# Performance work log

Measured on AMD Instinct MI355X. Metric: run time of the kernel, lower is better.

Reference implementation:

```python
import jax, jax.numpy as jnp
import numpy as np

B, T, C, H, N = 4, 4096, 2048, 32, 64
DMIX, DDEC = 32, 64
N_LAYER, LAYER_ID = 24, 12
GN_EPS = 1e-5 * 8.0 ** 2  # eps = 1e-5 * head_size_divisor**2


def setup_inputs() -> dict:
    key = jax.random.key(0)
    ks = jax.random.split(key, 24)
    r01 = LAYER_ID / (N_LAYER - 1)
    r1a0 = 1.0 - LAYER_ID / N_LAYER
    ddd = (np.arange(C, dtype=np.float32) / C).reshape(1, 1, C)
    maa = lambda p: jnp.asarray(1.0 - ddd ** p, dtype=jnp.float32)
    # decay speed schedule (canonical RWKV6, over channel dim)
    n = np.arange(C, dtype=np.float32)
    decay = (-6.0 + 5.0 * (n / (C - 1)) ** (0.7 + 1.3 * r01)).reshape(1, 1, C)
    # time_faaaa zigzag schedule
    m = np.arange(C, dtype=np.float32)
    zig = ((m + 1) % 3 - 1) * 0.1
    faaaa = (r01 * (1 - m / (C - 1)) + zig).reshape(H, N)
    s = 1.0 / np.sqrt(C)
    return {
        "x": jax.random.normal(ks[0], (B, T, C), jnp.float32),
        "shift_state": jax.random.normal(ks[1], (B, C), jnp.float32),
        "wkv_state": jnp.zeros((B, H, N, N), jnp.float32),
        "time_maa_x": maa(r1a0),
        "time_maa_w": maa(r1a0),
        "time_maa_k": maa(r1a0),
        "time_maa_v": jnp.asarray(1.0 - (ddd ** r1a0 + 0.3 * r01), jnp.float32),
        "time_maa_r": maa(0.5 * r1a0),
        "time_maa_g": maa(0.5 * r1a0),
        "time_maa_w1": jax.random.normal(ks[2], (C, 5 * DMIX), jnp.float32) * 0.01,
        "time_maa_w2": jax.random.uniform(ks[3], (5, DMIX, C), jnp.float32, -0.01, 0.01),
        "time_decay": jnp.asarray(decay, jnp.float32),
        "time_decay_w1": jax.random.normal(ks[4], (C, DDEC), jnp.float32) * 0.01,
        "time_decay_w2": jax.random.uniform(ks[5], (DDEC, C), jnp.float32, -0.01, 0.01),
        "time_faaaa": jnp.asarray(faaaa, jnp.float32),
        "Wr": jax.random.normal(ks[6], (C, C), jnp.float32) * s,
        "Wk": jax.random.normal(ks[7], (C, C), jnp.float32) * s,
        "Wv": jax.random.normal(ks[8], (C, C), jnp.float32) * s,
        "Wg": jax.random.normal(ks[9], (C, C), jnp.float32) * s,
        "Wo": jax.random.normal(ks[10], (C, C), jnp.float32) * s,
        "gn_weight": jnp.ones((C,), jnp.float32),
        "gn_bias": jnp.zeros((C,), jnp.float32),
    }


def reference(x, shift_state, wkv_state, time_maa_x, time_maa_w, time_maa_k,
              time_maa_v, time_maa_r, time_maa_g, time_maa_w1, time_maa_w2,
              time_decay, time_decay_w1, time_decay_w2, time_faaaa,
              Wr, Wk, Wv, Wg, Wo, gn_weight, gn_bias):
    b, t, c = x.shape
    # token shift: previous token (seeded by shift_state) minus current
    xx = jnp.concatenate([shift_state[:, None, :], x[:, :-1]], axis=1) - x
    lx = x[:, -1]
    # LoRA token-shift mixing
    xxx = x + xx * time_maa_x
    t5 = jnp.tanh(xxx @ time_maa_w1).reshape(b, t, 5, DMIX)
    mixes = jnp.einsum('btfd,fdc->fbtc', t5, time_maa_w2)
    mw, mk, mv, mr, mg = mixes
    xw = x + xx * (time_maa_w + mw)
    xk = x + xx * (time_maa_k + mk)
    xv = x + xx * (time_maa_v + mv)
    xr = x + xx * (time_maa_r + mr)
    xg = x + xx * (time_maa_g + mg)
    r = xr @ Wr
    k = xk @ Wk
    v = xv @ Wv
    g = jax.nn.silu(xg @ Wg)
    # data-dependent decay via LoRA; wkv6 uses log-decay -exp(w)
    w = time_decay + jnp.tanh(xw @ time_decay_w1) @ time_decay_w2
    glog = -jnp.exp(w)  # [b,t,c]
    to_heads = lambda z: z.reshape(b, t, H, N).transpose(1, 0, 2, 3)  # [t,b,h,n]
    rh, kh, vh, gh = to_heads(r), to_heads(k), to_heads(v), to_heads(glog)
    u = time_faaaa  # [H,N]

    def step(S, inp):
        r_t, k_t, v_t, g_t = inp  # each [b,h,n]
        kv = jnp.einsum('bhk,bhv->bhkv', k_t, v_t)
        o_t = jnp.einsum('bhk,bhkv->bhv', r_t, S + u[None, :, :, None] * kv)
        S = jnp.exp(g_t)[..., None] * S + kv
        return S, o_t

    state, o = jax.lax.scan(step, wkv_state, (rh, kh, vh, gh))
    o = o.transpose(1, 0, 2, 3).reshape(b, t, c)  # [b,t,c]
    # GroupNorm with H groups over channel dim
    og = o.reshape(b, t, H, N)
    mu = og.mean(-1, keepdims=True)
    var = og.var(-1, keepdims=True)
    on = (og - mu) * jax.lax.rsqrt(var + GN_EPS)
    on = on * gn_weight.reshape(H, N) + gn_bias.reshape(H, N)
    out = (on.reshape(b, t, c) * g) @ Wo
    return out, lx, state
```

## Files before the change

kernel.cpp:

```cpp
#include <hip/hip_runtime.h>
#include <hip/hip_bf16.h>
#include <stdint.h>

#define DEV __device__ __forceinline__

typedef __bf16 bf16x8 __attribute__((ext_vector_type(8)));
typedef float f32x4 __attribute__((ext_vector_type(4)));
typedef unsigned short u16x8 __attribute__((ext_vector_type(8)));

constexpr int kB = 4, kT = 4096, kC = 2048, kH = 32, kN = 64;
constexpr int kM = kB * kT;
constexpr int SEGN = 8, TSEG = kT / SEGN, CHN = TSEG / 64;

DEV float bfu2f(unsigned short u) {
  union { uint32_t i; float f; } x; x.i = ((uint32_t)u) << 16; return x.f;
}
DEV unsigned short f2bfu(float f) {
  union { float f; uint32_t i; } x; x.f = f;
  uint32_t r = x.i + 0x7FFFu + ((x.i >> 16) & 1u);
  return (unsigned short)(r >> 16);
}

DEV void gld16(const void* g, void* l) {
  __builtin_amdgcn_global_load_lds(
      (const __attribute__((address_space(1))) void*)g,
      (__attribute__((address_space(3))) void*)l, 16, 0, 0);
}

DEV int swzb(int row, int byteoff) { return (row << 7) + (byteoff ^ ((row & 7) << 4)); }
DEV int swz64(int row, int byteoff) { return (row << 6) + (byteoff ^ ((row & 3) << 4)); }

__global__ __launch_bounds__(256) void trans_bf16(
    const float* __restrict__ in, unsigned short* __restrict__ out, int R, int Cn) {
  __shared__ __attribute__((aligned(16))) unsigned short tile[64][65];
  const int t = threadIdx.x;
  const int r0 = blockIdx.y * 64, c0 = blockIdx.x * 64;
  const int lr = t >> 6, lc = t & 63;
#pragma unroll
  for (int i = 0; i < 16; i++) {
    int rr = lr + i * 4;
    int gr = r0 + rr, gc = c0 + lc;
    if (gr < R && gc < Cn) tile[rr][lc] = f2bfu(in[(size_t)gr * Cn + gc]);
  }
  __syncthreads();
#pragma unroll
  for (int i = 0; i < 16; i++) {
    int cc = lr + i * 4;
    int gc = c0 + cc, gr = r0 + lc;
    if (gc < Cn && gr < R) out[(size_t)gc * R + gr] = tile[lc][cc];
  }
}

__global__ __launch_bounds__(256) void prep_x2(
    const float* __restrict__ x, const float* __restrict__ shift,
    const float* __restrict__ maax,
    unsigned short* __restrict__ xxx, float* __restrict__ lx) {
  size_t i4 = ((size_t)blockIdx.x * 256 + threadIdx.x) * 4;
  int c = (int)(i4 & (kC - 1));
  size_t bt = i4 >> 11;
  int tt = (int)(bt & (kT - 1));
  int b = (int)(bt >> 12);
  float4 xv = *(const float4*)(x + i4);
  float4 pv = (tt == 0) ? *(const float4*)(shift + (size_t)b * kC + c)
                        : *(const float4*)(x + i4 - kC);
  float4 mx = *(const float4*)(maax + c);
  ushort4 o4;
  o4.x = f2bfu(xv.x + (pv.x - xv.x) * mx.x);
  o4.y = f2bfu(xv.y + (pv.y - xv.y) * mx.y);
  o4.z = f2bfu(xv.z + (pv.z - xv.z) * mx.z);
  o4.w = f2bfu(xv.w + (pv.w - xv.w) * mx.w);
  *(ushort4*)(xxx + i4) = o4;
  if (tt == kT - 1) *(float4*)(lx + (size_t)b * kC + c) = xv;
}

enum { E_F32 = 0, E_BF16 = 1, E_TANH = 2, E_SILU = 3 };

template <int BM, int BN, int EPI>
__global__ __launch_bounds__(256) void gemm_k(
    const unsigned short* __restrict__ A, const unsigned short* __restrict__ Bt,
    void* __restrict__ Cout, int M, int N, int K) {
  constexpr int WGM = (BM == 128 && BN == 128) ? 2 : (BM == 64 ? 2 : 4);
  constexpr int WGN = 4 / WGM;
  constexpr int WM = BM / WGM, WN = BN / WGN;
  constexpr int WR = WM / 16, WC = WN / 16;
  __shared__ __attribute__((aligned(16))) unsigned short As[BM * 32];
  __shared__ __attribute__((aligned(16))) unsigned short Bs[BN * 32];
  const int t = threadIdx.x, wid = t >> 6, l = t & 63;
  const int m0 = blockIdx.x * BM, n0 = blockIdx.y * BN;
  const int wm0 = (wid / WGN) * WM, wn0 = (wid % WGN) * WN;
  f32x4 acc[WR][WC];
#pragma unroll
  for (int i = 0; i < WR; i++)
#pragma unroll
    for (int j = 0; j < WC; j++) acc[i][j] = f32x4{0.f, 0.f, 0.f, 0.f};

  const int rowS = t >> 2, cbS = (t & 3) * 16;
  const char* Ab = (const char*)A;
  const char* Bb = (const char*)Bt;
  const int aoff = (wm0 + (l & 15)) * 32 + (l >> 4) * 8;
  const int boff = (wn0 + (l & 15)) * 32 + (l >> 4) * 8;

  for (int kt = 0; kt < K; kt += 32) {
#pragma unroll
    for (int ia = 0; ia < BM / 64; ia++)
      gld16(Ab + ((size_t)(m0 + ia * 64 + rowS) * K + kt) * 2 + cbS,
            (char*)As + ia * 4096 + wid * 1024);
    if constexpr (BN >= 64) {
#pragma unroll
      for (int ib = 0; ib < BN / 64; ib++)
        gld16(Bb + ((size_t)(n0 + ib * 64 + rowS) * K + kt) * 2 + cbS,
              (char*)Bs + ib * 4096 + wid * 1024);
    } else {
      if (t < BN * 4)
        gld16(Bb + ((size_t)(n0 + rowS) * K + kt) * 2 + cbS,
              (char*)Bs + wid * 1024);
    }
    __syncthreads();
    bf16x8 af[WR], bfv[WC];
#pragma unroll
    for (int mi = 0; mi < WR; mi++) af[mi] = *(const bf16x8*)(&As[aoff + mi * 512]);
#pragma unroll
    for (int ni = 0; ni < WC; ni++) bfv[ni] = *(const bf16x8*)(&Bs[boff + ni * 512]);
#pragma unroll
    for (int mi = 0; mi < WR; mi++)
#pragma unroll
      for (int ni = 0; ni < WC; ni++)
        acc[mi][ni] = __builtin_amdgcn_mfma_f32_16x16x32_bf16(af[mi], bfv[ni], acc[mi][ni], 0, 0, 0);
    __syncthreads();
  }

#pragma unroll
  for (int mi = 0; mi < WR; mi++) {
#pragma unroll
    for (int ni = 0; ni < WC; ni++) {
      int row = m0 + wm0 + mi * 16 + (l >> 4) * 4;
      int col = n0 + wn0 + ni * 16 + (l & 15);
#pragma unroll
      for (int j = 0; j < 4; j++) {
        float v = acc[mi][ni][j];
        size_t idx = (size_t)(row + j) * N + col;
        if constexpr (EPI == E_F32) ((float*)Cout)[idx] = v;
        else if constexpr (EPI == E_BF16) ((unsigned short*)Cout)[idx] = f2bfu(v);
        else if constexpr (EPI == E_TANH) ((unsigned short*)Cout)[idx] = f2bfu(tanhf(v));
        else if constexpr (EPI == E_SILU) ((unsigned short*)Cout)[idx] = f2bfu(v / (1.f + expf(-v)));
      }
    }
  }
}

template <int EPI>
__global__ __launch_bounds__(512, 2) void gemm256_k(
    const unsigned short* __restrict__ A, const unsigned short* __restrict__ Bt,
    void* __restrict__ Cout, int M, int N, int K) {
  extern __shared__ __attribute__((aligned(16))) char lds[];
  const int tid = threadIdx.x, wid = tid >> 6, l = tid & 63;
  const int fr = l & 15, fq = l >> 4;

  const int mtiles = M >> 8, ntiles = N >> 8;
  const int slab = mtiles >> 3;
  const int xcd = blockIdx.x & 7, loc = blockIdx.x >> 3;
  const int m0 = (xcd * slab + loc / ntiles) * 256;
  const int n0 = (loc % ntiles) * 256;

  const int wm = (wid >> 2) * 128, wn = (wid & 3) * 64;

  const int srow0 = tid >> 2;
  const int scb = ((tid & 3) * 16) ^ ((srow0 & 3) << 4);
  const char* pa2[2]; const char* pb2[2];
#pragma unroll
  for (int i = 0; i < 2; i++) {
    pa2[i] = (const char*)A + (size_t)(m0 + i * 128 + srow0) * K * 2 + scb;
    pb2[i] = (const char*)Bt + (size_t)(n0 + i * 128 + srow0) * K * 2 + scb;
  }

  const char* vA[8]; const char* vB[4];
#pragma unroll
  for (int mi = 0; mi < 8; mi++)
    vA[mi] = lds + swz64(wm + mi * 16 + fr, fq * 16);
#pragma unroll
  for (int ni = 0; ni < 4; ni++)
    vB[ni] = lds + 32768 + swz64(wn + ni * 16 + fr, fq * 16);

  f32x4 acc[8][4];
#pragma unroll
  for (int i = 0; i < 8; i++)
#pragma unroll
    for (int j = 0; j < 4; j++) acc[i][j] = f32x4{0.f, 0.f, 0.f, 0.f};

  auto STG = [&](int q, int s, int ktb) {
    const int d = q * 65536 + s * 16384 + wid * 1024;
    gld16(pa2[0] + ktb + s * 64, lds + d);
    gld16(pa2[1] + ktb + s * 64, lds + d + 8192);
    gld16(pb2[0] + ktb + s * 64, lds + 32768 + d);
    gld16(pb2[1] + ktb + s * 64, lds + 32768 + d + 8192);
  };

  auto PH = [&](int p, int s, bool doStage, int ktbNext, int vm) {
    if (vm)
      asm volatile("s_waitcnt vmcnt(4)" ::: "memory");
    else
      asm volatile("s_waitcnt vmcnt(0)" ::: "memory");
    __builtin_amdgcn_s_barrier();
    __builtin_amdgcn_sched_barrier(0);
    const int pb = p * 65536 + s * 16384;
    bf16x8 a[8], b[4];
#pragma unroll
    for (int mi = 0; mi < 8; mi++) a[mi] = *(const bf16x8*)(vA[mi] + pb);
#pragma unroll
    for (int ni = 0; ni < 4; ni++) b[ni] = *(const bf16x8*)(vB[ni] + pb);
    if (doStage) STG(p ^ 1, s, ktbNext);
    __builtin_amdgcn_sched_barrier(0);
    __builtin_amdgcn_s_setprio(1);
#pragma unroll
    for (int ni = 0; ni < 4; ni++)
#pragma unroll
      for (int mi = 0; mi < 8; mi++)
        acc[mi][ni] = __builtin_amdgcn_mfma_f32_16x16x32_bf16(a[mi], b[ni], acc[mi][ni], 0, 0, 0);
    __builtin_amdgcn_s_setprio(0);
  };

  const int KT = K >> 6;
  STG(0, 0, 0);
  STG(0, 1, 0);

  int T = 0;
  for (; T + 2 < KT; T += 2) {
    PH(0, 0, true, (T + 1) * 128, 4);
    PH(0, 1, true, (T + 1) * 128, 4);
    PH(1, 0, true, (T + 2) * 128, 4);
    PH(1, 1, true, (T + 2) * 128, 4);
  }
  PH(0, 0, true, (KT - 1) * 128, 4);
  PH(0, 1, true, (KT - 1) * 128, 4);
  PH(1, 0, false, 0, 4);
  PH(1, 1, false, 0, 0);

#pragma unroll
  for (int mi = 0; mi < 8; mi++)
#pragma unroll
    for (int ni = 0; ni < 4; ni++) {
      int row = m0 + wm + mi * 16 + fq * 4;
      int col = n0 + wn + ni * 16 + fr;
#pragma unroll
      for (int j = 0; j < 4; j++) {
        float v = acc[mi][ni][j];
        size_t idx = (size_t)(row + j) * N + col;
        if constexpr (EPI == E_F32) ((float*)Cout)[idx] = v;
        else if constexpr (EPI == E_BF16) ((unsigned short*)Cout)[idx] = f2bfu(v);
        else if constexpr (EPI == E_SILU) ((unsigned short*)Cout)[idx] = f2bfu(v / (1.f + expf(-v)));
      }
    }
}

__global__ __launch_bounds__(256) void mix4f_k(
    const unsigned short* __restrict__ t5, const unsigned short* __restrict__ w2t,
    const float* __restrict__ x, const float* __restrict__ shift,
    const float* __restrict__ maaw, const float* __restrict__ maak,
    const float* __restrict__ maav, const float* __restrict__ maar,
    unsigned short* __restrict__ xw, unsigned short* __restrict__ xk,
    unsigned short* __restrict__ xvo, unsigned short* __restrict__ xr) {
  __shared__ __attribute__((aligned(16))) char arena[32768];
  float* tile = (float*)arena;
  const int t = threadIdx.x, wid = t >> 6, l = t & 63;
  const int m0 = blockIdx.x * 64, n0 = blockIdx.y * 64;
  const int wm0 = (wid >> 1) * 32, wn0 = (wid & 1) * 32;
  const int rowS = t >> 2, cbS = (t & 3) * 16;
  const int fr = l & 15, fq = l >> 4;
  const int aoffB = ((wm0 + fr) * 32 + fq * 8) * 2;
  const int boffB = ((wn0 + fr) * 32 + fq * 8) * 2;

#pragma unroll
  for (int f = 0; f < 4; f++) {
    gld16((const char*)t5 + ((size_t)(m0 + rowS) * 160 + f * 32) * 2 + cbS, arena + f * 4096 + wid * 1024);
    gld16((const char*)w2t + ((size_t)(n0 + rowS) * 160 + f * 32) * 2 + cbS, arena + 16384 + f * 4096 + wid * 1024);
  }
  __syncthreads();
  f32x4 ac[4][2][2];
#pragma unroll
  for (int f = 0; f < 4; f++) {
    bf16x8 a0 = *(const bf16x8*)(arena + f * 4096 + aoffB);
    bf16x8 a1 = *(const bf16x8*)(arena + f * 4096 + aoffB + 1024);
    bf16x8 b0 = *(const bf16x8*)(arena + 16384 + f * 4096 + boffB);
    bf16x8 b1 = *(const bf16x8*)(arena + 16384 + f * 4096 + boffB + 1024);
    ac[f][0][0] = __builtin_amdgcn_mfma_f32_16x16x32_bf16(a0, b0, f32x4{0.f, 0.f, 0.f, 0.f}, 0, 0, 0);
    ac[f][0][1] = __builtin_amdgcn_mfma_f32_16x16x32_bf16(a0, b1, f32x4{0.f, 0.f, 0.f, 0.f}, 0, 0, 0);
    ac[f][1][0] = __builtin_amdgcn_mfma_f32_16x16x32_bf16(a1, b0, f32x4{0.f, 0.f, 0.f, 0.f}, 0, 0, 0);
    ac[f][1][1] = __builtin_amdgcn_mfma_f32_16x16x32_bf16(a1, b1, f32x4{0.f, 0.f, 0.f, 0.f}, 0, 0, 0);
  }

  const int rrow = m0 + (t >> 2);
  const int c0 = (t & 3) * 16;
  const size_t base = (size_t)rrow * kC + n0 + c0;
  float xreg[16], dreg[16];
  {
    const int tt = rrow & (kT - 1);
    const float* pvp = (tt == 0) ? (shift + (size_t)(rrow >> 12) * kC + n0 + c0)
                                 : (x + base - kC);
#pragma unroll
    for (int q = 0; q < 4; q++) {
      float4 xv4 = *(const float4*)(x + base + q * 4);
      float4 pv4 = *(const float4*)(pvp + q * 4);
      xreg[q * 4 + 0] = xv4.x; dreg[q * 4 + 0] = pv4.x - xv4.x;
      xreg[q * 4 + 1] = xv4.y; dreg[q * 4 + 1] = pv4.y - xv4.y;
      xreg[q * 4 + 2] = xv4.z; dreg[q * 4 + 2] = pv4.z - xv4.z;
      xreg[q * 4 + 3] = xv4.w; dreg[q * 4 + 3] = pv4.w - xv4.w;
    }
  }

  unsigned short* outs[4] = { xw, xk, xvo, xr };
  const float* maas[4] = { maaw, maak, maav, maar };
#pragma unroll
  for (int f = 0; f < 4; f++) {
    __syncthreads();
#pragma unroll
    for (int mi = 0; mi < 2; mi++)
#pragma unroll
      for (int ni = 0; ni < 2; ni++)
#pragma unroll
        for (int j = 0; j < 4; j++)
          tile[(wm0 + mi * 16 + fq * 4 + j) * 68 + wn0 + ni * 16 + fr] = ac[f][mi][ni][j];
    __syncthreads();
    const float* mp = maas[f] + n0 + c0;
    u16x8 o0, o1;
#pragma unroll
    for (int q = 0; q < 4; q++) {
      f32x4 m4 = *(const f32x4*)&tile[(t >> 2) * 68 + c0 + q * 4];
      float4 ma4 = *(const float4*)(mp + q * 4);
      float mv[4] = { ma4.x, ma4.y, ma4.z, ma4.w };
#pragma unroll
      for (int e = 0; e < 4; e++) {
        int i = q * 4 + e;
        unsigned short r = f2bfu(xreg[i] + dreg[i] * (mv[e] + m4[e]));
        if (i < 8) o0[i] = r; else o1[i - 8] = r;
      }
    }
    *(u16x8*)(outs[f] + base) = o0;
    *(u16x8*)(outs[f] + base + 8) = o1;
  }
}

__global__ __launch_bounds__(256) void mixf_k(
    const unsigned short* __restrict__ t5, const unsigned short* __restrict__ w2t,
    const float* __restrict__ x, const float* __restrict__ shift,
    const float* __restrict__ maa, unsigned short* __restrict__ xout, int f) {
  __shared__ __attribute__((aligned(16))) char arena[17408];
  float* tile = (float*)arena;
  const int t = threadIdx.x, wid = t >> 6, l = t & 63;
  const int m0 = blockIdx.x * 64, n0 = blockIdx.y * 64;
  const int wm0 = (wid >> 1) * 32, wn0 = (wid & 1) * 32;
  const int rowS = t >> 2, cbS = (t & 3) * 16;
  const int fr = l & 15, fq = l >> 4;
  const int aoffB = ((wm0 + fr) * 32 + fq * 8) * 2;
  const int boffB = ((wn0 + fr) * 32 + fq * 8) * 2;

  gld16((const char*)t5 + ((size_t)(m0 + rowS) * 160 + f * 32) * 2 + cbS, arena + wid * 1024);
  gld16((const char*)w2t + ((size_t)(n0 + rowS) * 160 + f * 32) * 2 + cbS, arena + 4096 + wid * 1024);
  __syncthreads();
  bf16x8 a0 = *(const bf16x8*)(arena + aoffB);
  bf16x8 a1 = *(const bf16x8*)(arena + aoffB + 1024);
  bf16x8 b0 = *(const bf16x8*)(arena + 4096 + boffB);
  bf16x8 b1 = *(const bf16x8*)(arena + 4096 + boffB + 1024);
  f32x4 ac[2][2];
  ac[0][0] = __builtin_amdgcn_mfma_f32_16x16x32_bf16(a0, b0, f32x4{0.f, 0.f, 0.f, 0.f}, 0, 0, 0);
  ac[0][1] = __builtin_amdgcn_mfma_f32_16x16x32_bf16(a0, b1, f32x4{0.f, 0.f, 0.f, 0.f}, 0, 0, 0);
  ac[1][0] = __builtin_amdgcn_mfma_f32_16x16x32_bf16(a1, b0, f32x4{0.f, 0.f, 0.f, 0.f}, 0, 0, 0);
  ac[1][1] = __builtin_amdgcn_mfma_f32_16x16x32_bf16(a1, b1, f32x4{0.f, 0.f, 0.f, 0.f}, 0, 0, 0);

  __syncthreads();
#pragma unroll
  for (int mi = 0; mi < 2; mi++)
#pragma unroll
    for (int ni = 0; ni < 2; ni++)
#pragma unroll
      for (int j = 0; j < 4; j++)
        tile[(wm0 + mi * 16 + fq * 4 + j) * 68 + wn0 + ni * 16 + fr] = ac[mi][ni][j];
  __syncthreads();

  const int rrow = m0 + (t >> 2);
  const int c0 = (t & 3) * 16;
  const size_t base = (size_t)rrow * kC + n0 + c0;
  const int tt = rrow & (kT - 1);
  const float* pvp = (tt == 0) ? (shift + (size_t)(rrow >> 12) * kC + n0 + c0)
                               : (x + base - kC);
  const float* mp = maa + n0 + c0;
  u16x8 o0, o1;
#pragma unroll
  for (int q = 0; q < 4; q++) {
    float4 xv4 = *(const float4*)(x + base + q * 4);
    float4 pv4 = *(const float4*)(pvp + q * 4);
    f32x4 m4 = *(const f32x4*)&tile[(t >> 2) * 68 + c0 + q * 4];
    float4 ma4 = *(const float4*)(mp + q * 4);
    float xe[4] = { xv4.x, xv4.y, xv4.z, xv4.w };
    float de[4] = { pv4.x - xv4.x, pv4.y - xv4.y, pv4.z - xv4.z, pv4.w - xv4.w };
    float me[4] = { ma4.x, ma4.y, ma4.z, ma4.w };
#pragma unroll
    for (int e = 0; e < 4; e++) {
      int i = q * 4 + e;
      unsigned short r = f2bfu(xe[e] + de[e] * (me[e] + m4[e]));
      if (i < 8) o0[i] = r; else o1[i - 8] = r;
    }
  }
  *(u16x8*)(xout + base) = o0;
  *(u16x8*)(xout + base + 8) = o1;
}

__global__ __launch_bounds__(256) void wkv_local_k(
    const unsigned short* __restrict__ kb, const unsigned short* __restrict__ vb,
    const unsigned short* __restrict__ dtmp, const unsigned short* __restrict__ td2t,
    const float* __restrict__ tdec,
    float* __restrict__ Lbuf, float* __restrict__ Dseg, float* __restrict__ edec) {
  const int bid = blockIdx.x;
  const int bh = bid >> 3, seg = bid & 7;
  const int h = bh & 31, b = bh >> 5;
  const int tid = threadIdx.x, w = tid >> 6, l = tid & 63;
  __shared__ __attribute__((aligned(16))) char arena[32768];
  char* KQks = arena;
  char* Vt   = arena + 8192;
  float* EdB = (float*)arena;
  char* TdB  = arena + 16384;
  char* DtA  = arena + 24576;
  __shared__ float segp[4][64];
  __shared__ float DLs[64];
  __shared__ float tdf[64];

  const int fr = l & 15, fq = l >> 4;
  f32x4 Sreg[4];
#pragma unroll
  for (int ni = 0; ni < 4; ni++) Sreg[ni] = f32x4{0.f, 0.f, 0.f, 0.f};

  {
    int r1 = tid >> 3, r2 = 32 + r1;
    int cb1 = ((tid & 7) * 16) ^ ((r1 & 7) << 4);
    int cb2 = ((tid & 7) * 16) ^ ((r2 & 7) << 4);
    gld16((const char*)td2t + (size_t)(h * 64 + r1) * 128 + cb1, TdB + w * 1024);
    gld16((const char*)td2t + (size_t)(h * 64 + r2) * 128 + cb2, TdB + 4096 + w * 1024);
    if (tid < 64) tdf[tid] = tdec[h * 64 + tid];
  }

  float dtot = 1.f;
  float kv[16], vv[16];
  {
    size_t g = ((size_t)b * kT + seg * TSEG + w * 16) * kC + h * 64 + l;
#pragma unroll
    for (int i = 0; i < 16; i++) {
      kv[i] = bfu2f(kb[g]); vv[i] = bfu2f(vb[g]);
      g += kC;
    }
  }

  for (int ch = 0; ch < CHN; ++ch) {
    const size_t gt0 = (size_t)b * kT + seg * TSEG + ch * 64;
    {
      int r1 = tid >> 3, r2 = 32 + r1;
      int cb1 = ((tid & 7) * 16) ^ ((r1 & 7) << 4);
      int cb2 = ((tid & 7) * 16) ^ ((r2 & 7) << 4);
      gld16((const char*)dtmp + (gt0 + r1) * 128 + cb1, DtA + w * 1024);
      gld16((const char*)dtmp + (gt0 + r2) * 128 + cb2, DtA + 4096 + w * 1024);
    }
    __syncthreads();

    f32x4 dacc[4];
    {
      bf16x8 af0 = *(const bf16x8*)(DtA + swzb(w * 16 + fr, fq * 16));
      bf16x8 af1 = *(const bf16x8*)(DtA + swzb(w * 16 + fr, fq * 16 + 64));
#pragma unroll
      for (int nj = 0; nj < 4; nj++) {
        bf16x8 b0 = *(const bf16x8*)(TdB + swzb(nj * 16 + fr, fq * 16));
        bf16x8 b1 = *(const bf16x8*)(TdB + swzb(nj * 16 + fr, fq * 16 + 64));
        dacc[nj] = __builtin_amdgcn_mfma_f32_16x16x32_bf16(af0, b0, f32x4{0.f, 0.f, 0.f, 0.f}, 0, 0, 0);
        dacc[nj] = __builtin_amdgcn_mfma_f32_16x16x32_bf16(af1, b1, dacc[nj], 0, 0, 0);
      }
    }
#pragma unroll
    for (int nj = 0; nj < 4; nj++) {
      float tv = tdf[nj * 16 + fr];
#pragma unroll
      for (int j = 0; j < 4; j++)
        EdB[(w * 16 + fq * 4 + j) * 64 + nj * 16 + fr] = expf(-expf(dacc[nj][j] + tv));
    }
    __syncthreads();

    float dvv[16];
    float p = 1.f;
    {
      size_t eg = (gt0 + w * 16) * kC + h * 64 + l;
#pragma unroll
      for (int i = 0; i < 16; i++) {
        float d = EdB[(w * 16 + i) * 64 + l];
        dvv[i] = d; p *= d;
        edec[eg] = d; eg += kC;
      }
    }
    segp[w][l] = p;
    __syncthreads();

    float pre = 1.f;
    if (w > 0) pre *= segp[0][l];
    if (w > 1) pre *= segp[1][l];
    if (w > 2) pre *= segp[2][l];
    if (w == 3) DLs[l] = pre * p;

    unsigned short kqrow[16], vtrow[16];
    float run = pre;
#pragma unroll
    for (int i = 0; i < 16; i++) {
      run *= dvv[i];
      kqrow[i] = f2bfu(kv[i] / run);
      vtrow[i] = f2bfu(vv[i]);
    }
    {
      u16x8 q0, q1, v0, v1;
#pragma unroll
      for (int j = 0; j < 8; j++) { q0[j] = kqrow[j]; q1[j] = kqrow[j + 8]; v0[j] = vtrow[j]; v1[j] = vtrow[j + 8]; }
      *(u16x8*)(KQks + swzb(l, w * 32)) = q0;
      *(u16x8*)(KQks + swzb(l, w * 32 + 16)) = q1;
      *(u16x8*)(Vt + swzb(l, w * 32)) = v0;
      *(u16x8*)(Vt + swzb(l, w * 32 + 16)) = v1;
    }
    if (ch < CHN - 1) {
      size_t g = ((size_t)b * kT + seg * TSEG + (ch + 1) * 64 + w * 16) * kC + h * 64 + l;
#pragma unroll
      for (int i = 0; i < 16; i++) {
        kv[i] = bfu2f(kb[g]); vv[i] = bfu2f(vb[g]);
        g += kC;
      }
    }
    __syncthreads();

    bf16x8 kA0 = *(const bf16x8*)(KQks + swzb(w * 16 + fr, fq * 16));
    bf16x8 kA1 = *(const bf16x8*)(KQks + swzb(w * 16 + fr, fq * 16 + 64));
    f32x4 kvacc[4];
#pragma unroll
    for (int ni = 0; ni < 4; ni++) {
      bf16x8 bv0 = *(const bf16x8*)(Vt + swzb(ni * 16 + fr, fq * 16));
      bf16x8 bv1 = *(const bf16x8*)(Vt + swzb(ni * 16 + fr, fq * 16 + 64));
      kvacc[ni] = __builtin_amdgcn_mfma_f32_16x16x32_bf16(kA0, bv0, f32x4{0.f, 0.f, 0.f, 0.f}, 0, 0, 0);
      kvacc[ni] = __builtin_amdgcn_mfma_f32_16x16x32_bf16(kA1, bv1, kvacc[ni], 0, 0, 0);
    }
    float dlj[4];
#pragma unroll
    for (int j = 0; j < 4; j++) dlj[j] = DLs[w * 16 + fq * 4 + j];
#pragma unroll
    for (int ni = 0; ni < 4; ni++)
#pragma unroll
      for (int j = 0; j < 4; j++)
        Sreg[ni][j] = (Sreg[ni][j] + kvacc[ni][j]) * dlj[j];
    dtot *= DLs[l];
  }

  float* Lp = Lbuf + (size_t)bid * 4096;
#pragma unroll
  for (int ni = 0; ni < 4; ni++)
#pragma unroll
    for (int j = 0; j < 4; j++)
      Lp[(size_t)(w * 16 + fq * 4 + j) * 64 + ni * 16 + fr] = Sreg[ni][j];
  if (w == 0) Dseg[(size_t)bid * 64 + l] = dtot;
}

__global__ __launch_bounds__(256) void wkv_combine_k(
    const float* __restrict__ s0, const float* __restrict__ Dseg,
    float* __restrict__ Lbuf, float* __restrict__ sOut) {
  const int bh = blockIdx.x, tid = threadIdx.x;
  const int k = tid >> 2, v0 = (tid & 3) * 16;
  float4 s[4];
  const float* sp = s0 + (size_t)bh * 4096 + (size_t)k * 64 + v0;
#pragma unroll
  for (int q = 0; q < 4; q++) s[q] = ((const float4*)sp)[q];
  for (int seg = 0; seg < SEGN; ++seg) {
    size_t idx = (size_t)bh * SEGN + seg;
    float d = Dseg[idx * 64 + k];
    float* Lp = Lbuf + idx * 4096 + (size_t)k * 64 + v0;
#pragma unroll
    for (int q = 0; q < 4; q++) {
      float4 lq = ((float4*)Lp)[q];
      ((float4*)Lp)[q] = s[q];
      s[q].x = d * s[q].x + lq.x; s[q].y = d * s[q].y + lq.y;
      s[q].z = d * s[q].z + lq.z; s[q].w = d * s[q].w + lq.w;
    }
  }
  float* op = sOut + (size_t)bh * 4096 + (size_t)k * 64 + v0;
#pragma unroll
  for (int q = 0; q < 4; q++) ((float4*)op)[q] = s[q];
}

__global__ __launch_bounds__(256) void wkv_seg_k(
    const unsigned short* __restrict__ rb, const unsigned short* __restrict__ kb,
    const unsigned short* __restrict__ vb, const float* __restrict__ ed,
    const float* __restrict__ uf, const float* __restrict__ Sini,
    unsigned short* __restrict__ o) {
  const int bid = blockIdx.x;
  const int bh = bid >> 3, seg = bid & 7;
  const int h = bh & 31, b = bh >> 5;
  const int tid = threadIdx.x, w = tid >> 6, l = tid & 63;
  __shared__ __attribute__((aligned(16))) unsigned short RQ[4096];
  __shared__ __attribute__((aligned(16))) unsigned short KQsk[4096];
  __shared__ __attribute__((aligned(16))) unsigned short KQks[4096];
  __shared__ __attribute__((aligned(16))) unsigned short Vt[4096];
  __shared__ __attribute__((aligned(16))) unsigned short Pl[4096];
  __shared__ __attribute__((aligned(16))) unsigned short S0T[4096];
  __shared__ __attribute__((aligned(16))) unsigned short RU[4096];
  __shared__ __attribute__((aligned(16))) unsigned short Ksk[4096];
  __shared__ float segp[4][64];
  __shared__ float DLs[64];

  const float uu = uf[h * 64 + l];
  const int fr = l & 15, fq = l >> 4;

  f32x4 Sreg[4];
#pragma unroll
  for (int ni = 0; ni < 4; ni++)
#pragma unroll
    for (int j = 0; j < 4; j++) {
      int kk2 = w * 16 + fq * 4 + j, vv2 = ni * 16 + fr;
      float sv = Sini[(size_t)bid * 4096 + (size_t)kk2 * 64 + vv2];
      Sreg[ni][j] = sv;
      *(unsigned short*)((char*)S0T + swzb(vv2, kk2 * 2)) = f2bfu(sv);
    }
  __syncthreads();

  float rv[16], kv[16], dv[16], vv[16];
  {
    size_t g = ((size_t)b * kT + seg * TSEG + w * 16) * kC + h * 64 + l;
#pragma unroll
    for (int i = 0; i < 16; i++) {
      rv[i] = bfu2f(rb[g]); kv[i] = bfu2f(kb[g]); vv[i] = bfu2f(vb[g]); dv[i] = ed[g];
      g += kC;
    }
  }

  for (int ch = 0; ch < CHN; ++ch) {
    float p = 1.f;
#pragma unroll
    for (int i = 0; i < 16; i++) p *= dv[i];
    segp[w][l] = p;
    __syncthreads();
    float pre = 1.f;
    if (w > 0) pre *= segp[0][l];
    if (w > 1) pre *= segp[1][l];
    if (w > 2) pre *= segp[2][l];
    if (w == 3) DLs[l] = pre * p;

    unsigned short kqrow[16], vtrow[16];
    float run = pre;
#pragma unroll
    for (int i = 0; i < 16; i++) {
      int t = w * 16 + i;
      float rq = rv[i] * run;
      run *= dv[i];
      float kq = kv[i] / run;
      *(unsigned short*)((char*)RQ + swzb(t, l * 2)) = f2bfu(rq);
      *(unsigned short*)((char*)RU + swzb(t, l * 2)) = f2bfu(rv[i] * uu);
      *(unsigned short*)((char*)Ksk + swzb(t, l * 2)) = f2bfu(kv[i]);
      unsigned short kqu = f2bfu(kq);
      *(unsigned short*)((char*)KQsk + swzb(t, l * 2)) = kqu;
      kqrow[i] = kqu;
      vtrow[i] = f2bfu(vv[i]);
    }
    {
      u16x8 q0, q1, v0, v1;
#pragma unroll
      for (int j = 0; j < 8; j++) { q0[j] = kqrow[j]; q1[j] = kqrow[j + 8]; v0[j] = vtrow[j]; v1[j] = vtrow[j + 8]; }
      *(u16x8*)((char*)KQks + swzb(l, w * 32)) = q0;
      *(u16x8*)((char*)KQks + swzb(l, w * 32 + 16)) = q1;
      *(u16x8*)((char*)Vt + swzb(l, w * 32)) = v0;
      *(u16x8*)((char*)Vt + swzb(l, w * 32 + 16)) = v1;
    }

    if (ch < CHN - 1) {
      size_t g = ((size_t)b * kT + seg * TSEG + (ch + 1) * 64 + w * 16) * kC + h * 64 + l;
#pragma unroll
      for (int i = 0; i < 16; i++) {
        rv[i] = bfu2f(rb[g]); kv[i] = bfu2f(kb[g]); vv[i] = bfu2f(vb[g]); dv[i] = ed[g];
        g += kC;
      }
    }
    __syncthreads();

    bf16x8 a0 = *(const bf16x8*)((const char*)RQ + swzb(w * 16 + fr, fq * 16));
    bf16x8 a1 = *(const bf16x8*)((const char*)RQ + swzb(w * 16 + fr, fq * 16 + 64));
    f32x4 pacc[4];
#pragma unroll
    for (int ni = 0; ni < 4; ni++) {
      bf16x8 b0 = *(const bf16x8*)((const char*)KQsk + swzb(ni * 16 + fr, fq * 16));
      bf16x8 b1 = *(const bf16x8*)((const char*)KQsk + swzb(ni * 16 + fr, fq * 16 + 64));
      pacc[ni] = __builtin_amdgcn_mfma_f32_16x16x32_bf16(a0, b0, f32x4{0.f, 0.f, 0.f, 0.f}, 0, 0, 0);
      pacc[ni] = __builtin_amdgcn_mfma_f32_16x16x32_bf16(a1, b1, pacc[ni], 0, 0, 0);
    }
    f32x4 dacc;
    {
      bf16x8 ru0 = *(const bf16x8*)((const char*)RU + swzb(w * 16 + fr, fq * 16));
      bf16x8 ru1 = *(const bf16x8*)((const char*)RU + swzb(w * 16 + fr, fq * 16 + 64));
      bf16x8 kb0 = *(const bf16x8*)((const char*)Ksk + swzb(w * 16 + fr, fq * 16));
      bf16x8 kb1 = *(const bf16x8*)((const char*)Ksk + swzb(w * 16 + fr, fq * 16 + 64));
      dacc = __builtin_amdgcn_mfma_f32_16x16x32_bf16(ru0, kb0, f32x4{0.f, 0.f, 0.f, 0.f}, 0, 0, 0);
      dacc = __builtin_amdgcn_mfma_f32_16x16x32_bf16(ru1, kb1, dacc, 0, 0, 0);
    }
    float dg[4];
#pragma unroll
    for (int j = 0; j < 4; j++) dg[j] = __shfl(dacc[j], fq * 20 + j, 64);
#pragma unroll
    for (int ni = 0; ni < 4; ni++)
#pragma unroll
      for (int j = 0; j < 4; j++) {
        int row = w * 16 + fq * 4 + j, col = ni * 16 + fr;
        float pv = pacc[ni][j];
        pv = (col < row) ? pv : ((col == row) ? dg[j] : 0.f);
        *(unsigned short*)((char*)Pl + swzb(row, col * 2)) = f2bfu(pv);
      }
    __syncthreads();

    bf16x8 pA0 = *(const bf16x8*)((const char*)Pl + swzb(w * 16 + fr, fq * 16));
    bf16x8 pA1 = *(const bf16x8*)((const char*)Pl + swzb(w * 16 + fr, fq * 16 + 64));
    bf16x8 kA0 = *(const bf16x8*)((const char*)KQks + swzb(w * 16 + fr, fq * 16));
    bf16x8 kA1 = *(const bf16x8*)((const char*)KQks + swzb(w * 16 + fr, fq * 16 + 64));
    f32x4 oacc[4], kvacc[4];
#pragma unroll
    for (int ni = 0; ni < 4; ni++) {
      bf16x8 bv0 = *(const bf16x8*)((const char*)Vt + swzb(ni * 16 + fr, fq * 16));
      bf16x8 bv1 = *(const bf16x8*)((const char*)Vt + swzb(ni * 16 + fr, fq * 16 + 64));
      bf16x8 bs0 = *(const bf16x8*)((const char*)S0T + swzb(ni * 16 + fr, fq * 16));
      bf16x8 bs1 = *(const bf16x8*)((const char*)S0T + swzb(ni * 16 + fr, fq * 16 + 64));
      oacc[ni] = __builtin_amdgcn_mfma_f32_16x16x32_bf16(pA0, bv0, f32x4{0.f, 0.f, 0.f, 0.f}, 0, 0, 0);
      oacc[ni] = __builtin_amdgcn_mfma_f32_16x16x32_bf16(pA1, bv1, oacc[ni], 0, 0, 0);
      oacc[ni] = __builtin_amdgcn_mfma_f32_16x16x32_bf16(a0, bs0, oacc[ni], 0, 0, 0);
      oacc[ni] = __builtin_amdgcn_mfma_f32_16x16x32_bf16(a1, bs1, oacc[ni], 0, 0, 0);
      kvacc[ni] = __builtin_amdgcn_mfma_f32_16x16x32_bf16(kA0, bv0, f32x4{0.f, 0.f, 0.f, 0.f}, 0, 0, 0);
      kvacc[ni] = __builtin_amdgcn_mfma_f32_16x16x32_bf16(kA1, bv1, kvacc[ni], 0, 0, 0);
    }
    size_t obase = ((size_t)b * kT + seg * TSEG + ch * 64) * kC + h * 64;
#pragma unroll
    for (int ni = 0; ni < 4; ni++)
#pragma unroll
      for (int j = 0; j < 4; j++)
        o[obase + (size_t)(w * 16 + fq * 4 + j) * kC + ni * 16 + fr] = f2bfu(oacc[ni][j]);
    __syncthreads();

    float dlj[4];
#pragma unroll
    for (int j = 0; j < 4; j++) dlj[j] = DLs[w * 16 + fq * 4 + j];
#pragma unroll
    for (int ni = 0; ni < 4; ni++)
#pragma unroll
      for (int j = 0; j < 4; j++) {
        int kk2 = w * 16 + fq * 4 + j, vv2 = ni * 16 + fr;
        float sn = (Sreg[ni][j] + kvacc[ni][j]) * dlj[j];
        Sreg[ni][j] = sn;
        *(unsigned short*)((char*)S0T + swzb(vv2, kk2 * 2)) = f2bfu(sn);
      }
  }
}

__global__ __launch_bounds__(256) void gn_k(
    const unsigned short* __restrict__ o, const unsigned short* __restrict__ gb,
    const float* __restrict__ gnw, const float* __restrict__ gnb,
    unsigned short* __restrict__ y) {
  int gi = blockIdx.x * 4 + (threadIdx.x >> 6);
  int j = threadIdx.x & 63;
  int bt = gi >> 5, h = gi & 31;
  size_t idx = (size_t)bt * kC + h * 64 + j;
  float val = bfu2f(o[idx]);
  float s = val, s2 = val * val;
#pragma unroll
  for (int m = 1; m < 64; m <<= 1) {
    s += __shfl_xor(s, m, 64);
    s2 += __shfl_xor(s2, m, 64);
  }
  float mu = s * 0.015625f;
  float var = s2 * 0.015625f - mu * mu;
  float rs = rsqrtf(var + 6.4e-4f);
  float on = (val - mu) * rs * gnw[h * 64 + j] + gnb[h * 64 + j];
  y[idx] = f2bfu(on * bfu2f(gb[idx]));
}

constexpr size_t SZW     = (size_t)2048 * 2048 * 2;
constexpr size_t OFF_WRT = 0;
constexpr size_t OFF_WKT = 1 * SZW;
constexpr size_t OFF_WVT = 2 * SZW;
constexpr size_t OFF_WGT = 3 * SZW;
constexpr size_t OFF_WOT = 4 * SZW;
constexpr size_t OFF_W1T = 5 * SZW;
constexpr size_t OFF_W2T = OFF_W1T + (size_t)160 * 2048 * 2;
constexpr size_t OFF_TD1 = OFF_W2T + (size_t)2048 * 160 * 2;
constexpr size_t OFF_TD2 = OFF_TD1 + (size_t)64 * 2048 * 2;
constexpr size_t OFF_T5  = OFF_TD2 + (size_t)2048 * 64 * 2;
constexpr size_t OFF_DT  = OFF_T5 + (size_t)kM * 160 * 2;
constexpr size_t OFF_EDEC= OFF_DT + (size_t)kM * 64 * 2;
constexpr size_t OFF_X   = OFF_EDEC + (size_t)kM * kC * 4;
constexpr size_t OFF_R   = OFF_X + (size_t)kM * kC * 2;
constexpr size_t OFF_K   = OFF_R + (size_t)kM * kC * 2;
constexpr size_t OFF_V   = OFF_K + (size_t)kM * kC * 2;
constexpr size_t OFF_L   = OFF_WRT;

extern "C" void kernel_launch(void* const* d_in, const int* in_sizes, int n_in,
                              void* d_out, int out_size, void* d_ws, size_t ws_size,
                              hipStream_t stream) {
  const float* x     = (const float*)d_in[0];
  const float* shift = (const float*)d_in[1];
  const float* s0    = (const float*)d_in[2];
  const float* maax  = (const float*)d_in[3];
  const float* maaw  = (const float*)d_in[4];
  const float* maak  = (const float*)d_in[5];
  const float* maav  = (const float*)d_in[6];
  const float* maar  = (const float*)d_in[7];
  const float* maag  = (const float*)d_in[8];
  const float* w1    = (const float*)d_in[9];
  const float* w2    = (const float*)d_in[10];
  const float* tdec  = (const float*)d_in[11];
  const float* tdw1  = (const float*)d_in[12];
  const float* tdw2  = (const float*)d_in[13];
  const float* faaaa = (const float*)d_in[14];
  const float* Wr    = (const float*)d_in[15];
  const float* Wk    = (const float*)d_in[16];
  const float* Wv    = (const float*)d_in[17];
  const float* Wg    = (const float*)d_in[18];
  const float* Wo    = (const float*)d_in[19];
  const float* gnw   = (const float*)d_in[20];
  const float* gnb   = (const float*)d_in[21];

  char* ws = (char*)d_ws;
  unsigned short* Wrt  = (unsigned short*)(ws + OFF_WRT);
  unsigned short* Wkt  = (unsigned short*)(ws + OFF_WKT);
  unsigned short* Wvt  = (unsigned short*)(ws + OFF_WVT);
  unsigned short* Wgt  = (unsigned short*)(ws + OFF_WGT);
  unsigned short* Wot  = (unsigned short*)(ws + OFF_WOT);
  unsigned short* w1t  = (unsigned short*)(ws + OFF_W1T);
  unsigned short* w2t  = (unsigned short*)(ws + OFF_W2T);
  unsigned short* td1t = (unsigned short*)(ws + OFF_TD1);
  unsigned short* td2t = (unsigned short*)(ws + OFF_TD2);
  unsigned short* t5   = (unsigned short*)(ws + OFF_T5);
  unsigned short* dtmp = (unsigned short*)(ws + OFF_DT);
  float*          edec = (float*)(ws + OFF_EDEC);
  unsigned short* xg   = (unsigned short*)(ws + OFF_EDEC);
  unsigned short* bufX = (unsigned short*)(ws + OFF_X);
  unsigned short* bufR = (unsigned short*)(ws + OFF_R);
  unsigned short* bufK = (unsigned short*)(ws + OFF_K);
  unsigned short* bufV = (unsigned short*)(ws + OFF_V);
  float*          Lbuf = (float*)(ws + OFF_L);
  float*          DsegP= (float*)(ws + OFF_TD1);

  float* outp  = (float*)d_out;
  float* lx    = outp + (size_t)kM * kC;
  float* stOut = lx + (size_t)kB * kC;

  dim3 blk(256);

  trans_bf16<<<dim3(32, 32), blk, 0, stream>>>(Wr, Wrt, 2048, 2048);
  trans_bf16<<<dim3(32, 32), blk, 0, stream>>>(Wk, Wkt, 2048, 2048);
  trans_bf16<<<dim3(32, 32), blk, 0, stream>>>(Wv, Wvt, 2048, 2048);
  trans_bf16<<<dim3(32, 32), blk, 0, stream>>>(Wg, Wgt, 2048, 2048);
  trans_bf16<<<dim3(32, 32), blk, 0, stream>>>(Wo, Wot, 2048, 2048);
  trans_bf16<<<dim3(3, 32), blk, 0, stream>>>(w1, w1t, 2048, 160);
  trans_bf16<<<dim3(1, 32), blk, 0, stream>>>(tdw1, td1t, 2048, 64);
  trans_bf16<<<dim3(32, 1), blk, 0, stream>>>(tdw2, td2t, 64, 2048);
  trans_bf16<<<dim3(32, 3), blk, 0, stream>>>(w2, w2t, 160, 2048);

  prep_x2<<<dim3(kM * kC / 4 / 256), blk, 0, stream>>>(x, shift, maax, bufX, lx);

  gemm_k<128, 32, E_TANH><<<dim3(kM / 128, 5), blk, 0, stream>>>(bufX, w1t, t5, kM, 160, 2048);

  dim3 mgrid(kM / 64, kC / 64);
  constexpr int G256 = (kM / 256) * (kC / 256);
  constexpr size_t LDS256 = 131072;

  mix4f_k<<<mgrid, blk, 0, stream>>>(t5, w2t, x, shift, maaw, maak, maav, maar,
                                     bufX, bufV, bufR, bufK);
  gemm_k<64, 64, E_TANH><<<dim3(kM / 64, 1), blk, 0, stream>>>(bufX, td1t, dtmp, kM, 64, 2048);

  gemm256_k<E_BF16><<<dim3(G256), dim3(512), LDS256, stream>>>(bufV, Wkt, bufX, kM, 2048, 2048);
  gemm256_k<E_BF16><<<dim3(G256), dim3(512), LDS256, stream>>>(bufR, Wvt, bufV, kM, 2048, 2048);
  gemm256_k<E_BF16><<<dim3(G256), dim3(512), LDS256, stream>>>(bufK, Wrt, bufR, kM, 2048, 2048);

  wkv_local_k<<<dim3(kB * kH * SEGN), blk, 0, stream>>>(bufX, bufV, dtmp, td2t, tdec,
                                                        Lbuf, DsegP, edec);
  wkv_combine_k<<<dim3(kB * kH), blk, 0, stream>>>(s0, DsegP, Lbuf, stOut);
  wkv_seg_k<<<dim3(kB * kH * SEGN), blk, 0, stream>>>(bufR, bufX, bufV, edec, faaaa, Lbuf, bufK);

  mixf_k<<<mgrid, blk, 0, stream>>>(t5, w2t, x, shift, maag, xg, 4);
  gemm256_k<E_SILU><<<dim3(G256), dim3(512), LDS256, stream>>>(xg, Wgt, bufX, kM, 2048, 2048);

  gn_k<<<dim3(kM * kH / 4), blk, 0, stream>>>(bufK, bufX, gnw, gnb, bufV);

  gemm256_k<E_F32><<<dim3(G256), dim3(512), LDS256, stream>>>(bufV, Wot, outp, kM, 2048, 2048);
}
```

Before: 1.444 ms.

## Recompute decay inside wkv_seg_k instead of storing an fp32 edec buffer

Result: no change. 1.437 ms (-0.5%).

```diff
diff --git a/kernel.cpp b/kernel.cpp
--- a/kernel.cpp
+++ b/kernel.cpp
@@ -408,7 +408,7 @@
     const unsigned short* __restrict__ kb, const unsigned short* __restrict__ vb,
     const unsigned short* __restrict__ dtmp, const unsigned short* __restrict__ td2t,
     const float* __restrict__ tdec,
-    float* __restrict__ Lbuf, float* __restrict__ Dseg, float* __restrict__ edec) {
+    float* __restrict__ Lbuf, float* __restrict__ Dseg) {
   const int bid = blockIdx.x;
   const int bh = bid >> 3, seg = bid & 7;
   const int h = bh & 31, b = bh >> 5;
@@ -478,18 +478,12 @@
       for (int j = 0; j < 4; j++)
         EdB[(w * 16 + fq * 4 + j) * 64 + nj * 16 + fr] = expf(-expf(dacc[nj][j] + tv));
     }
-    __syncthreads();
-
     float dvv[16];
     float p = 1.f;
-    {
-      size_t eg = (gt0 + w * 16) * kC + h * 64 + l;
-#pragma unroll
-      for (int i = 0; i < 16; i++) {
-        float d = EdB[(w * 16 + i) * 64 + l];
-        dvv[i] = d; p *= d;
-        edec[eg] = d; eg += kC;
-      }
+#pragma unroll
+    for (int i = 0; i < 16; i++) {
+      float d = EdB[(w * 16 + i) * 64 + l];
+      dvv[i] = d; p *= d;
     }
     segp[w][l] = p;
     __syncthreads();
@@ -585,26 +579,34 @@
 
 __global__ __launch_bounds__(256) void wkv_seg_k(
     const unsigned short* __restrict__ rb, const unsigned short* __restrict__ kb,
-    const unsigned short* __restrict__ vb, const float* __restrict__ ed,
+    const unsigned short* __restrict__ vb,
+    const unsigned short* __restrict__ dtmp, const unsigned short* __restrict__ td2t,
+    const float* __restrict__ tdec,
     const float* __restrict__ uf, const float* __restrict__ Sini,
     unsigned short* __restrict__ o) {
   const int bid = blockIdx.x;
   const int bh = bid >> 3, seg = bid & 7;
   const int h = bh & 31, b = bh >> 5;
   const int tid = threadIdx.x, w = tid >> 6, l = tid & 63;
-  __shared__ __attribute__((aligned(16))) unsigned short RQ[4096];
-  __shared__ __attribute__((aligned(16))) unsigned short KQsk[4096];
-  __shared__ __attribute__((aligned(16))) unsigned short KQks[4096];
-  __shared__ __attribute__((aligned(16))) unsigned short Vt[4096];
-  __shared__ __attribute__((aligned(16))) unsigned short Pl[4096];
-  __shared__ __attribute__((aligned(16))) unsigned short S0T[4096];
-  __shared__ __attribute__((aligned(16))) unsigned short RU[4096];
-  __shared__ __attribute__((aligned(16))) unsigned short Ksk[4096];
+  __shared__ __attribute__((aligned(16))) char arena[65536];
+  char* RQ   = arena;
+  char* KQsk = arena + 8192;
+  char* KQks = arena + 16384;
+  char* Vt   = arena + 24576;
+  char* Pl   = arena + 32768;
+  char* S0T  = arena + 40960;
+  char* RU   = arena + 49152;
+  char* Ksk  = arena + 57344;
+  float* EdB = (float*)arena;
+  char* DtA  = RU;
+  char* TdB  = Ksk;
   __shared__ float segp[4][64];
   __shared__ float DLs[64];
+  __shared__ float tdf[64];
 
   const float uu = uf[h * 64 + l];
   const int fr = l & 15, fq = l >> 4;
+  if (tid < 64) tdf[tid] = tdec[h * 64 + tid];
 
   f32x4 Sreg[4];
 #pragma unroll
@@ -614,26 +616,61 @@
       int kk2 = w * 16 + fq * 4 + j, vv2 = ni * 16 + fr;
       float sv = Sini[(size_t)bid * 4096 + (size_t)kk2 * 64 + vv2];
       Sreg[ni][j] = sv;
-      *(unsigned short*)((char*)S0T + swzb(vv2, kk2 * 2)) = f2bfu(sv);
+      *(unsigned short*)(S0T + swzb(vv2, kk2 * 2)) = f2bfu(sv);
     }
   __syncthreads();
 
-  float rv[16], kv[16], dv[16], vv[16];
+  float rv[16], kv[16], vv[16];
   {
     size_t g = ((size_t)b * kT + seg * TSEG + w * 16) * kC + h * 64 + l;
 #pragma unroll
     for (int i = 0; i < 16; i++) {
-      rv[i] = bfu2f(rb[g]); kv[i] = bfu2f(kb[g]); vv[i] = bfu2f(vb[g]); dv[i] = ed[g];
+      rv[i] = bfu2f(rb[g]); kv[i] = bfu2f(kb[g]); vv[i] = bfu2f(vb[g]);
       g += kC;
     }
   }
 
+  const int r1s = tid >> 3, r2s = 32 + r1s;
+  const int cb1 = ((tid & 7) * 16) ^ ((r1s & 7) << 4);
+  const int cb2 = ((tid & 7) * 16) ^ ((r2s & 7) << 4);
+
   for (int ch = 0; ch < CHN; ++ch) {
+    const size_t gt0 = (size_t)b * kT + seg * TSEG + ch * 64;
+    gld16((const char*)dtmp + (gt0 + r1s) * 128 + cb1, DtA + w * 1024);
+    gld16((const char*)dtmp + (gt0 + r2s) * 128 + cb2, DtA + 4096 + w * 1024);
+    gld16((const char*)td2t + (size_t)(h * 64 + r1s) * 128 + cb1, TdB + w * 1024);
+    gld16((const char*)td2t + (size_t)(h * 64 + r2s) * 128 + cb2, TdB + 4096 + w * 1024);
+    __syncthreads();
+
+    f32x4 dacc[4];
+    {
+      bf16x8 af0 = *(const bf16x8*)(DtA + swzb(w * 16 + fr, fq * 16));
+      bf16x8 af1 = *(const bf16x8*)(DtA + swzb(w * 16 + fr, fq * 16 + 64));
+#pragma unroll
+      for (int nj = 0; nj < 4; nj++) {
+        bf16x8 b0 = *(const bf16x8*)(TdB + swzb(nj * 16 + fr, fq * 16));
+        bf16x8 b1 = *(const bf16x8*)(TdB + swzb(nj * 16 + fr, fq * 16 + 64));
+        dacc[nj] = __builtin_amdgcn_mfma_f32_16x16x32_bf16(af0, b0, f32x4{0.f, 0.f, 0.f, 0.f}, 0, 0, 0);
+        dacc[nj] = __builtin_amdgcn_mfma_f32_16x16x32_bf16(af1, b1, dacc[nj], 0, 0, 0);
+      }
+    }
+#pragma unroll
+    for (int nj = 0; nj < 4; nj++) {
+      float tv = tdf[nj * 16 + fr];
+#pragma unroll
+      for (int j = 0; j < 4; j++)
+        EdB[(w * 16 + fq * 4 + j) * 64 + nj * 16 + fr] = expf(-expf(dacc[nj][j] + tv));
+    }
+    float dv[16];
     float p = 1.f;
 #pragma unroll
-    for (int i = 0; i < 16; i++) p *= dv[i];
+    for (int i = 0; i < 16; i++) {
+      dv[i] = EdB[(w * 16 + i) * 64 + l];
+      p *= dv[i];
+    }
     segp[w][l] = p;
     __syncthreads();
+
     float pre = 1.f;
     if (w > 0) pre *= segp[0][l];
     if (w > 1) pre *= segp[1][l];
@@ -648,11 +685,11 @@
       float rq = rv[i] * run;
       run *= dv[i];
       float kq = kv[i] / run;
-      *(unsigned short*)((char*)RQ + swzb(t, l * 2)) = f2bfu(rq);
-      *(unsigned short*)((char*)RU + swzb(t, l * 2)) = f2bfu(rv[i] * uu);
-      *(unsigned short*)((char*)Ksk + swzb(t, l * 2)) = f2bfu(kv[i]);
+      *(unsigned short*)(RQ + swzb(t, l * 2)) = f2bfu(rq);
+      *(unsigned short*)(RU + swzb(t, l * 2)) = f2bfu(rv[i] * uu);
+      *(unsigned short*)(Ksk + swzb(t, l * 2)) = f2bfu(kv[i]);
       unsigned short kqu = f2bfu(kq);
-      *(unsigned short*)((char*)KQsk + swzb(t, l * 2)) = kqu;
+      *(unsigned short*)(KQsk + swzb(t, l * 2)) = kqu;
       kqrow[i] = kqu;
       vtrow[i] = f2bfu(vv[i]);
     }
@@ -660,44 +697,44 @@
       u16x8 q0, q1, v0, v1;
 #pragma unroll
       for (int j = 0; j < 8; j++) { q0[j] = kqrow[j]; q1[j] = kqrow[j + 8]; v0[j] = vtrow[j]; v1[j] = vtrow[j + 8]; }
-      *(u16x8*)((char*)KQks + swzb(l, w * 32)) = q0;
-      *(u16x8*)((char*)KQks + swzb(l, w * 32 + 16)) = q1;
-      *(u16x8*)((char*)Vt + swzb(l, w * 32)) = v0;
-      *(u16x8*)((char*)Vt + swzb(l, w * 32 + 16)) = v1;
+      *(u16x8*)(KQks + swzb(l, w * 32)) = q0;
+      *(u16x8*)(KQks + swzb(l, w * 32 + 16)) = q1;
+      *(u16x8*)(Vt + swzb(l, w * 32)) = v0;
+      *(u16x8*)(Vt + swzb(l, w * 32 + 16)) = v1;
     }
 
     if (ch < CHN - 1) {
       size_t g = ((size_t)b * kT + seg * TSEG + (ch + 1) * 64 + w * 16) * kC + h * 64 + l;
 #pragma unroll
       for (int i = 0; i < 16; i++) {
-        rv[i] = bfu2f(rb[g]); kv[i] = bfu2f(kb[g]); vv[i] = bfu2f(vb[g]); dv[i] = ed[g];
+        rv[i] = bfu2f(rb[g]); kv[i] = bfu2f(kb[g]); vv[i] = bfu2f(vb[g]);
         g += kC;
       }
     }
     __syncthreads();
 
-    bf16x8 a0 = *(const bf16x8*)((const char*)RQ + swzb(w * 16 + fr, fq * 16));
-    bf16x8 a1 = *(const bf16x8*)((const char*)RQ + swzb(w * 16 + fr, fq * 16 + 64));
+    bf16x8 a0 = *(const bf16x8*)(RQ + swzb(w * 16 + fr, fq * 16));
+    bf16x8 a1 = *(const bf16x8*)(RQ + swzb(w * 16 + fr, fq * 16 + 64));
     f32x4 pacc[4];
 #pragma unroll
     for (int ni = 0; ni < 4; ni++) {
-      bf16x8 b0 = *(const bf16x8*)((const char*)KQsk + swzb(ni * 16 + fr, fq * 16));
-      bf16x8 b1 = *(const bf16x8*)((const char*)KQsk + swzb(ni * 16 + fr, fq * 16 + 64));
+      bf16x8 b0 = *(const bf16x8*)(KQsk + swzb(ni * 16 + fr, fq * 16));
+      bf16x8 b1 = *(const bf16x8*)(KQsk + swzb(ni * 16 + fr, fq * 16 + 64));
       pacc[ni] = __builtin_amdgcn_mfma_f32_16x16x32_bf16(a0, b0, f32x4{0.f, 0.f, 0.f, 0.f}, 0, 0, 0);
       pacc[ni] = __builtin_amdgcn_mfma_f32_16x16x32_bf16(a1, b1, pacc[ni], 0, 0, 0);
     }
-    f32x4 dacc;
+    f32x4 dacc2;
     {
-      bf16x8 ru0 = *(const bf16x8*)((const char*)RU + swzb(w * 16 + fr, fq * 16));
-      bf16x8 ru1 = *(const bf16x8*)((const char*)RU + swzb(w * 16 + fr, fq * 16 + 64));
-      bf16x8 kb0 = *(const bf16x8*)((const char*)Ksk + swzb(w * 16 + fr, fq * 16));
-      bf16x8 kb1 = *(const bf16x8*)((const char*)Ksk + swzb(w * 16 + fr, fq * 16 + 64));
-      dacc = __builtin_amdgcn_mfma_f32_16x16x32_bf16(ru0, kb0, f32x4{0.f, 0.f, 0.f, 0.f}, 0, 0, 0);
-      dacc = __builtin_amdgcn_mfma_f32_16x16x32_bf16(ru1, kb1, dacc, 0, 0, 0);
+      bf16x8 ru0 = *(const bf16x8*)(RU + swzb(w * 16 + fr, fq * 16));
+      bf16x8 ru1 = *(const bf16x8*)(RU + swzb(w * 16 + fr, fq * 16 + 64));
+      bf16x8 kb0 = *(const bf16x8*)(Ksk + swzb(w * 16 + fr, fq * 16));
+      bf16x8 kb1 = *(const bf16x8*)(Ksk + swzb(w * 16 + fr, fq * 16 + 64));
+      dacc2 = __builtin_amdgcn_mfma_f32_16x16x32_bf16(ru0, kb0, f32x4{0.f, 0.f, 0.f, 0.f}, 0, 0, 0);
+      dacc2 = __builtin_amdgcn_mfma_f32_16x16x32_bf16(ru1, kb1, dacc2, 0, 0, 0);
     }
     float dg[4];
 #pragma unroll
-    for (int j = 0; j < 4; j++) dg[j] = __shfl(dacc[j], fq * 20 + j, 64);
+    for (int j = 0; j < 4; j++) dg[j] = __shfl(dacc2[j], fq * 20 + j, 64);
 #pragma unroll
     for (int ni = 0; ni < 4; ni++)
 #pragma unroll
@@ -705,21 +742,21 @@
         int row = w * 16 + fq * 4 + j, col = ni * 16 + fr;
         float pv = pacc[ni][j];
         pv = (col < row) ? pv : ((col == row) ? dg[j] : 0.f);
-        *(unsigned short*)((char*)Pl + swzb(row, col * 2)) = f2bfu(pv);
+        *(unsigned short*)(Pl + swzb(row, col * 2)) = f2bfu(pv);
       }
     __syncthreads();
 
-    bf16x8 pA0 = *(const bf16x8*)((const char*)Pl + swzb(w * 16 + fr, fq * 16));
-    bf16x8 pA1 = *(const bf16x8*)((const char*)Pl + swzb(w * 16 + fr, fq * 16 + 64));
-    bf16x8 kA0 = *(const bf16x8*)((const char*)KQks + swzb(w * 16 + fr, fq * 16));
-    bf16x8 kA1 = *(const bf16x8*)((const char*)KQks + swzb(w * 16 + fr, fq * 16 + 64));
+    bf16x8 pA0 = *(const bf16x8*)(Pl + swzb(w * 16 + fr, fq * 16));
+    bf16x8 pA1 = *(const bf16x8*)(Pl + swzb(w * 16 + fr, fq * 16 + 64));
+    bf16x8 kA0 = *(const bf16x8*)(KQks + swzb(w * 16 + fr, fq * 16));
+    bf16x8 kA1 = *(const bf16x8*)(KQks + swzb(w * 16 + fr, fq * 16 + 64));
     f32x4 oacc[4], kvacc[4];
 #pragma unroll
     for (int ni = 0; ni < 4; ni++) {
-      bf16x8 bv0 = *(const bf16x8*)((const char*)Vt + swzb(ni * 16 + fr, fq * 16));
-      bf16x8 bv1 = *(const bf16x8*)((const char*)Vt + swzb(ni * 16 + fr, fq * 16 + 64));
-      bf16x8 bs0 = *(const bf16x8*)((const char*)S0T + swzb(ni * 16 + fr, fq * 16));
-      bf16x8 bs1 = *(const bf16x8*)((const char*)S0T + swzb(ni * 16 + fr, fq * 16 + 64));
+      bf16x8 bv0 = *(const bf16x8*)(Vt + swzb(ni * 16 + fr, fq * 16));
+      bf16x8 bv1 = *(const bf16x8*)(Vt + swzb(ni * 16 + fr, fq * 16 + 64));
+      bf16x8 bs0 = *(const bf16x8*)(S0T + swzb(ni * 16 + fr, fq * 16));
+      bf16x8 bs1 = *(const bf16x8*)(S0T + swzb(ni * 16 + fr, fq * 16 + 64));
       oacc[ni] = __builtin_amdgcn_mfma_f32_16x16x32_bf16(pA0, bv0, f32x4{0.f, 0.f, 0.f, 0.f}, 0, 0, 0);
       oacc[ni] = __builtin_amdgcn_mfma_f32_16x16x32_bf16(pA1, bv1, oacc[ni], 0, 0, 0);
       oacc[ni] = __builtin_amdgcn_mfma_f32_16x16x32_bf16(a0, bs0, oacc[ni], 0, 0, 0);
@@ -727,7 +764,7 @@
       kvacc[ni] = __builtin_amdgcn_mfma_f32_16x16x32_bf16(kA0, bv0, f32x4{0.f, 0.f, 0.f, 0.f}, 0, 0, 0);
       kvacc[ni] = __builtin_amdgcn_mfma_f32_16x16x32_bf16(kA1, bv1, kvacc[ni], 0, 0, 0);
     }
-    size_t obase = ((size_t)b * kT + seg * TSEG + ch * 64) * kC + h * 64;
+    size_t obase = gt0 * kC + h * 64;
 #pragma unroll
     for (int ni = 0; ni < 4; ni++)
 #pragma unroll
@@ -745,7 +782,7 @@
         int kk2 = w * 16 + fq * 4 + j, vv2 = ni * 16 + fr;
         float sn = (Sreg[ni][j] + kvacc[ni][j]) * dlj[j];
         Sreg[ni][j] = sn;
-        *(unsigned short*)((char*)S0T + swzb(vv2, kk2 * 2)) = f2bfu(sn);
+        *(unsigned short*)(S0T + swzb(vv2, kk2 * 2)) = f2bfu(sn);
       }
   }
 }
@@ -784,8 +821,8 @@
 constexpr size_t OFF_TD2 = OFF_TD1 + (size_t)64 * 2048 * 2;
 constexpr size_t OFF_T5  = OFF_TD2 + (size_t)2048 * 64 * 2;
 constexpr size_t OFF_DT  = OFF_T5 + (size_t)kM * 160 * 2;
-constexpr size_t OFF_EDEC= OFF_DT + (size_t)kM * 64 * 2;
-constexpr size_t OFF_X   = OFF_EDEC + (size_t)kM * kC * 4;
+constexpr size_t OFF_XG  = OFF_DT + (size_t)kM * 64 * 2;
+constexpr size_t OFF_X   = OFF_XG + (size_t)kM * kC * 4;
 constexpr size_t OFF_R   = OFF_X + (size_t)kM * kC * 2;
 constexpr size_t OFF_K   = OFF_R + (size_t)kM * kC * 2;
 constexpr size_t OFF_V   = OFF_K + (size_t)kM * kC * 2;
@@ -829,8 +866,7 @@
   unsigned short* td2t = (unsigned short*)(ws + OFF_TD2);
   unsigned short* t5   = (unsigned short*)(ws + OFF_T5);
   unsigned short* dtmp = (unsigned short*)(ws + OFF_DT);
-  float*          edec = (float*)(ws + OFF_EDEC);
-  unsigned short* xg   = (unsigned short*)(ws + OFF_EDEC);
+  unsigned short* xg   = (unsigned short*)(ws + OFF_XG);
   unsigned short* bufX = (unsigned short*)(ws + OFF_X);
   unsigned short* bufR = (unsigned short*)(ws + OFF_R);
   unsigned short* bufK = (unsigned short*)(ws + OFF_K);
@@ -871,9 +907,10 @@
   gemm256_k<E_BF16><<<dim3(G256), dim3(512), LDS256, stream>>>(bufK, Wrt, bufR, kM, 2048, 2048);
 
   wkv_local_k<<<dim3(kB * kH * SEGN), blk, 0, stream>>>(bufX, bufV, dtmp, td2t, tdec,
-                                                        Lbuf, DsegP, edec);
+                                                        Lbuf, DsegP);
   wkv_combine_k<<<dim3(kB * kH), blk, 0, stream>>>(s0, DsegP, Lbuf, stOut);
-  wkv_seg_k<<<dim3(kB * kH * SEGN), blk, 0, stream>>>(bufR, bufX, bufV, edec, faaaa, Lbuf, bufK);
+  wkv_seg_k<<<dim3(kB * kH * SEGN), blk, 0, stream>>>(bufR, bufX, bufV, dtmp, td2t, tdec,
+                                                      faaaa, Lbuf, bufK);
 
   mixf_k<<<mgrid, blk, 0, stream>>>(t5, w2t, x, shift, maag, xg, 4);
   gemm256_k<E_SILU><<<dim3(G256), dim3(512), LDS256, stream>>>(xg, Wgt, bufX, kM, 2048, 2048);
```
